# Kernel optimization log

Measured on AMD Instinct MI355X. Metric: run time of the kernel, lower is better.

The kernel has to match this reference:

```python
import jax, jax.numpy as jnp
import numpy as np

H = 12          # num_attention_heads
HD = 64         # head_dim
GAMMA = 0.5
LOCAL_EPS = 0.8
N_APPROX = 7


def _l1norm(x, axis):
    # torch.nn.functional.normalize(x, p=1, dim=axis)
    n = jnp.sum(jnp.abs(x), axis=axis, keepdims=True)
    return x / jnp.maximum(n, 1e-12)


def setup_inputs() -> dict:
    key = jax.random.key(0)
    ks = jax.random.split(key, 6)
    B, S, E = 2, 512, 768
    std = 1.0 / np.sqrt(E)
    hidden_states = jax.random.normal(ks[0], (B, S, E), jnp.float32)
    Wq = jax.random.normal(ks[1], (E, E), jnp.float32) * std
    Wk = jax.random.normal(ks[2], (E, E), jnp.float32) * std
    Wv = jax.random.normal(ks[3], (E, E), jnp.float32) * std
    bq = jnp.zeros((E,), jnp.float32)
    bk = jnp.zeros((E,), jnp.float32)
    bv = jnp.zeros((E,), jnp.float32)
    g = jax.random.randint(ks[4], (B * S, B * S), 0, 2, jnp.int32)
    attention_mask = jnp.zeros((B, S), jnp.float32)
    return {"hidden_states": hidden_states, "Wq": Wq, "bq": bq, "Wk": Wk,
            "bk": bk, "Wv": Wv, "bv": bv, "g": g,
            "attention_mask": attention_mask}


def reference(hidden_states, Wq, bq, Wk, bk, Wv, bv, g, attention_mask):
    B, S, E = hidden_states.shape
    BN = B * S
    x = hidden_states  # torch flattens batch-major: token index = b*S + s
    q = (x @ Wq + bq) / jnp.sqrt(jnp.float32(HD))
    k = x @ Wk + bk
    v = x @ Wv + bv
    # [B,S,E] -> [BN,H,HD] -> [H,BN,HD]
    q = q.reshape(BN, H, HD).transpose(1, 0, 2)
    k = k.reshape(BN, H, HD).transpose(1, 0, 2)
    v = v.reshape(BN, H, HD).transpose(1, 0, 2)

    # W_G[h,i,j] = exp(k_i . q_j)
    W_G = jnp.exp(jnp.einsum('hid,hjd->hij', k, q))

    # sparsification mask combined with token mask
    bool_mask = (attention_mask >= 0).reshape(-1).astype(jnp.int32)  # [BN]
    g_eff = g * (bool_mask[:, None] * bool_mask[None, :])
    W_G = jnp.where(g_eff > 0, W_G, jnp.zeros((), W_G.dtype))

    out_degree = W_G.sum(axis=2)                       # [H, BN]
    rhos = jax.lax.stop_gradient(out_degree.max(axis=1))  # [H]

    eye = jnp.eye(BN, dtype=W_G.dtype)
    Bmat = rhos[:, None, None] * eye + W_G - out_degree[:, :, None] * eye

    B_power = jnp.broadcast_to(eye, (H, BN, BN))
    L_gamma = jnp.broadcast_to(eye, (H, BN, BN))
    num = 1.0
    den = jnp.ones((H,), W_G.dtype)
    for ii in range(1, N_APPROX + 1):  # fixed 7-term power series
        num = num * (GAMMA - ii + 1) * -1.0
        den = den * (ii * rhos)
        coef = num / den                               # [H]
        B_power = jnp.einsum('hij,hjk->hik', Bmat, B_power)
        L_gamma = L_gamma + coef[:, None, None] * B_power
    L_gamma = L_gamma * (rhos[:, None, None] ** GAMMA)
    diags = jnp.diagonal(L_gamma, axis1=-2, axis2=-1)  # [H, BN]
    L_gamma = _l1norm(diags[:, :, None] * eye - L_gamma, axis=2)

    attn = (LOCAL_EPS * jnp.einsum('hij,hjd->hid', _l1norm(W_G, 2), v)
            + (1.0 - LOCAL_EPS) * jnp.einsum('hij,hjd->hid', L_gamma, v))

    # faithful to torch: raw reshape of [H,BN,HD] into [B,S,H,HD]
    out = attn.reshape(B, S, H, HD)
    out = jnp.swapaxes(out, 0, 1).reshape(S, B, E)
    return jnp.swapaxes(out, 0, 1)
```

## Files before the change

kernel.cpp:

```cpp
#include <hip/hip_runtime.h>
#include <hip/hip_bf16.h>

typedef __attribute__((ext_vector_type(4))) float f32x4;
typedef __attribute__((ext_vector_type(8))) short s16x8;

typedef const __attribute__((address_space(1))) void* gptr_t;
typedef __attribute__((address_space(3))) void* lptr_t;

__device__ __forceinline__ short f2b(float f){ __hip_bfloat16 h=__float2bfloat16(f); return *(short*)&h; }
__device__ __forceinline__ float b2f(short s){ __hip_bfloat16 h; *(short*)&h = s; return __bfloat162float(h); }

__device__ __forceinline__ void gl_lds16(const void* g, void* l){
  __builtin_amdgcn_global_load_lds((gptr_t)g, (lptr_t)l, 16, 0, 0);
}


__global__ __launch_bounds__(256) void cvt_x(const float* __restrict__ X, short* __restrict__ Xb){
  int i = blockIdx.x*256 + threadIdx.x;
  const float4* p = (const float4*)(X + (size_t)i*8);
  float4 a = p[0], b = p[1];
  s16x8 o;
  o[0]=f2b(a.x); o[1]=f2b(a.y); o[2]=f2b(a.z); o[3]=f2b(a.w);
  o[4]=f2b(b.x); o[5]=f2b(b.y); o[6]=f2b(b.z); o[7]=f2b(b.w);
  *(s16x8*)(Xb + (size_t)i*8) = o;
}

__global__ __launch_bounds__(256) void cvt_wt3(const float* __restrict__ Wq, const float* __restrict__ Wk,
      const float* __restrict__ Wv, short* __restrict__ WT){
  __shared__ short tile[64][72];
  int mat = blockIdx.x / 144; int bx = blockIdx.x % 144;
  const float* W = mat==0?Wq:(mat==1?Wk:Wv);
  short* O = WT + (size_t)mat*768*768;
  int bl = bx % 12, bn = bx / 12;
  int l0 = bl*64, n0 = bn*64;
  int t = threadIdx.x;
  #pragma unroll
  for (int p=0;p<4;p++){
    int lr = p*16 + (t>>4);
    int nc = (t&15)*4;
    float4 v = *(const float4*)(W + (size_t)(l0+lr)*768 + n0 + nc);
    tile[lr][nc+0]=f2b(v.x); tile[lr][nc+1]=f2b(v.y); tile[lr][nc+2]=f2b(v.z); tile[lr][nc+3]=f2b(v.w);
  }
  __syncthreads();
  #pragma unroll
  for (int p=0;p<2;p++){
    int nr = p*32 + (t>>3);
    int lc = (t&7)*8;
    s16x8 o;
    #pragma unroll
    for(int u=0;u<8;u++) o[u] = tile[lc+u][nr];
    *(s16x8*)(O + (size_t)(n0+nr)*768 + l0 + lc) = o;
  }
}

__global__ __launch_bounds__(256) void gpack(const int* __restrict__ g, unsigned* __restrict__ gb){
  int w = blockIdx.x*256 + threadIdx.x;
  const int* p = g + (size_t)w*32;
  unsigned b=0;
  #pragma unroll
  for(int i=0;i<32;i++) b |= (p[i]>0 ? 1u:0u) << i;
  gb[w]=b;
}

__global__ __launch_bounds__(256) void vtrans(const short* __restrict__ vs, short* __restrict__ vT){
  __shared__ short tile[64][72];
  int h = blockIdx.y; int i0 = blockIdx.x*64;
  int t = threadIdx.x;
  #pragma unroll
  for(int p=0;p<2;p++){
    int ir = p*32 + (t>>3); int c8=(t&7)*8;
    *(s16x8*)&tile[ir][c8] = *(const s16x8*)(vs + (size_t)(i0+ir)*768 + h*64 + c8);
  }
  __syncthreads();
  #pragma unroll
  for(int p=0;p<2;p++){
    int dr = p*32 + (t>>3); int i8=(t&7)*8;
    s16x8 o;
    #pragma unroll
    for(int u=0;u<8;u++) o[u]=tile[i8+u][dr];
    *(s16x8*)(vT + ((size_t)h*64 + dr)*1024 + i0 + i8) = o;
  }
}

__global__ __launch_bounds__(256) void qkv_gemm(const short* __restrict__ Xb, const short* __restrict__ WT,
      const float* __restrict__ bq, const float* __restrict__ bk, const float* __restrict__ bv,
      short* __restrict__ qs, short* __restrict__ ks, short* __restrict__ vs){
  __shared__ short lA[128*32], lB[128*32];
  int mat = blockIdx.y;
  const short* B = WT + (size_t)mat*768*768;
  const float* bias = mat==0?bq:(mat==1?bk:bv);
  short* outp = mat==0?qs:(mat==1?ks:vs);
  float scale = mat==0 ? 0.125f : 1.0f;
  int tm = (blockIdx.x / 6)*128, tn = (blockIdx.x % 6)*128;
  int t=threadIdx.x, wave=t>>6, lane=t&63;
  int srow=t>>2, scol=(t&3)*8;
  int wm=(wave>>1)*64, wn=(wave&1)*64;
  f32x4 acc[4][4]={};
  for (int k0=0;k0<768;k0+=32){
    #pragma unroll
    for(int r=0;r<2;++r){
      gl_lds16(Xb + (size_t)(tm+srow+r*64)*768 + k0 + scol, lA + r*2048 + wave*512);
      gl_lds16(B  + (size_t)(tn+srow+r*64)*768 + k0 + scol, lB + r*2048 + wave*512);
    }
    __syncthreads();
    int krow=(lane>>4)*8, rl=lane&15;
    s16x8 af[4], bfr[4];
    #pragma unroll
    for(int m=0;m<4;m++) af[m] = *(s16x8*)&lA[(wm+m*16+rl)*32 + krow];
    #pragma unroll
    for(int n=0;n<4;n++) bfr[n] = *(s16x8*)&lB[(wn+n*16+rl)*32 + krow];
    #pragma unroll
    for(int m=0;m<4;m++)
      #pragma unroll
      for(int n=0;n<4;n++)
        acc[m][n]=__builtin_amdgcn_mfma_f32_16x16x32_bf16(af[m],bfr[n],acc[m][n],0,0,0);
    __syncthreads();
  }
  int r0 = tm + wm + (lane>>4)*4, c0 = tn + wn + (lane&15);
  #pragma unroll
  for(int m=0;m<4;m++)
    #pragma unroll
    for(int n=0;n<4;n++){
      int col = c0 + n*16; float bb = bias[col];
      #pragma unroll
      for(int r=0;r<4;r++){
        int row = r0 + m*16 + r;
        outp[(size_t)row*768 + col] = f2b((acc[m][n][r] + bb)*scale);
      }
    }
}

__global__ __launch_bounds__(256) void wg_gemm(const short* __restrict__ kb, const short* __restrict__ qb,
      const unsigned* __restrict__ gb, const float* __restrict__ am,
      short* __restrict__ WG, float* __restrict__ od){
  __shared__ short lK[128*64], lQ[128*64];
  int h=blockIdx.y;
  int tm=(blockIdx.x>>3)*128, tn=(blockIdx.x&7)*128;
  int t=threadIdx.x, wave=t>>6, lane=t&63;
  int srow=t>>3, scol=(t&7)*8;
  int wm=(wave>>1)*64, wn=(wave&1)*64;
  #pragma unroll
  for(int r=0;r<4;++r){
    gl_lds16(kb + (size_t)(tm+srow+r*32)*768 + h*64 + scol, lK + r*2048 + wave*512);
    gl_lds16(qb + (size_t)(tn+srow+r*32)*768 + h*64 + scol, lQ + r*2048 + wave*512);
  }
  __syncthreads();
  int rl=lane&15;
  f32x4 acc[4][4]={};
  #pragma unroll
  for(int ks=0;ks<2;ks++){
    int krow=ks*32+(lane>>4)*8;
    s16x8 af[4], bfr[4];
    #pragma unroll
    for(int m=0;m<4;m++) af[m]=*(s16x8*)&lK[(wm+m*16+rl)*64+krow];
    #pragma unroll
    for(int n=0;n<4;n++) bfr[n]=*(s16x8*)&lQ[(wn+n*16+rl)*64+krow];
    #pragma unroll
    for(int m=0;m<4;m++)
      #pragma unroll
      for(int n=0;n<4;n++)
        acc[m][n]=__builtin_amdgcn_mfma_f32_16x16x32_bf16(af[m],bfr[n],acc[m][n],0,0,0);
  }
  size_t hm=(size_t)h<<20;
  int r0=tm+wm+(lane>>4)*4, c0=tn+wn+rl;
  #pragma unroll
  for(int m=0;m<4;m++){
    float rs[4]={0.f,0.f,0.f,0.f};
    #pragma unroll
    for(int n=0;n<4;n++){
      int col=c0+n*16;
      bool mc = am[col] >= 0.0f;
      unsigned sh = col & 31; int wofs = col >> 5;
      #pragma unroll
      for(int r=0;r<4;r++){
        int row=r0+m*16+r;
        float e = __expf(acc[m][n][r]);
        bool gbit = (gb[(row<<5) + wofs] >> sh) & 1u;
        float w = (gbit && am[row]>=0.0f && mc) ? e : 0.f;
        WG[hm+(size_t)row*1024+col]=f2b(w);
        rs[r]+=w;
      }
    }
    #pragma unroll
    for(int r=0;r<4;r++){
      float s=rs[r];
      #pragma unroll
      for(int off=1;off<16;off<<=1) s+=__shfl_xor(s,off);
      if(rl==0) atomicAdd(&od[(h<<10)+r0+m*16+r], s);
    }
  }
}

__global__ void rhos_k(const float* __restrict__ od, float* __restrict__ rhos){
  __shared__ float red[256];
  int h = blockIdx.x, t = threadIdx.x;
  float m = -1e30f;
  for (int i=t;i<1024;i+=256) m = fmaxf(m, od[(h<<10)+i]);
  red[t]=m; __syncthreads();
  for(int s=128;s>0;s>>=1){ if(t<s) red[t]=fmaxf(red[t],red[t+s]); __syncthreads(); }
  if(t==0) rhos[h]=red[0];
}

__global__ __launch_bounds__(256) void amat_t(const short* __restrict__ WG, const float* __restrict__ od,
      const float* __restrict__ rhos, short* __restrict__ Am, short* __restrict__ AmT,
      short* __restrict__ T){
  __shared__ short tile[64][72];
  const float b7 = -33.f/2048.f, b6 = -21.f/1024.f;
  int h = blockIdx.y; int bx = blockIdx.x;
  int rb = bx >> 4, cb = bx & 15;
  int r0 = rb*64, c0 = cb*64;
  float rho = rhos[h]; float inv = 1.0f/fmaxf(rho,1e-30f);
  size_t hm = (size_t)h<<20;
  int t = threadIdx.x;
  #pragma unroll
  for(int p=0;p<2;p++){
    int r = p*32 + (t>>3); int c8 = (t&7)*8;
    size_t base = hm + (size_t)(r0+r)*1024 + c0 + c8;
    s16x8 w = *(const s16x8*)(WG + base);
    s16x8 oa, ot;
    float dadd = (rho - od[(h<<10)+r0+r])*inv;
    #pragma unroll
    for(int u=0;u<8;u++){
      bool dg = (rb==cb) && ((c8+u)==r);
      float a = b2f(w[u])*inv + (dg ? dadd : 0.f);
      oa[u]=f2b(a);
      ot[u]=f2b(b7*a + (dg ? b6 : 0.f));
      tile[r][c8+u]=oa[u];
    }
    *(s16x8*)(Am+base)=oa; *(s16x8*)(T+base)=ot;
  }
  __syncthreads();
  #pragma unroll
  for(int p=0;p<2;p++){
    int c = p*32 + (t>>3); int r8 = (t&7)*8;
    s16x8 o;
    #pragma unroll
    for(int u=0;u<8;u++) o[u]=tile[r8+u][c];
    *(s16x8*)(AmT + hm + (size_t)(c0+c)*1024 + r0 + r8) = o;
  }
}

#define GEMM2P_PROLOG \
  __shared__ short lA[2][4096], lB[2][4096]; \
  int wg = ((int)blockIdx.x & 7)*96 + ((int)blockIdx.x >> 3); \
  int h = wg >> 6; int tile = wg & 63; \
  int tm=(tile>>3)*128, tn=(tile&7)*128; \
  size_t hm=(size_t)h<<20; \
  const short* Ag = A + hm; const short* Bg = B + hm; \
  int t=threadIdx.x, wave=t>>6, lane=t&63; \
  int srow=t>>2, scol=(t&3)*8; \
  int wm=(wave>>1)*64, wn=(wave&1)*64; \
  int krow=(lane>>4)*8, rl=lane&15; \
  const short* pA0 = Ag + (size_t)(tm+srow)*1024 + scol; \
  const short* pA1 = pA0 + (size_t)64*1024; \
  const short* pB0 = Bg + (size_t)(tn+srow)*1024 + scol; \
  const short* pB1 = pB0 + (size_t)64*1024; \
  f32x4 acc[4][4]={}; \
  gl_lds16(pA0, &lA[0][wave*512]); \
  gl_lds16(pA1, &lA[0][2048 + wave*512]); \
  gl_lds16(pB0, &lB[0][wave*512]); \
  gl_lds16(pB1, &lB[0][2048 + wave*512]); \
  pA0+=32; pA1+=32; pB0+=32; pB1+=32; \
  __syncthreads(); \
  int cur=0; \
  _Pragma("unroll 1") \
  for(int k0=32;k0<1024;k0+=32){ \
    gl_lds16(pA0, &lA[cur^1][wave*512]); \
    gl_lds16(pA1, &lA[cur^1][2048 + wave*512]); \
    gl_lds16(pB0, &lB[cur^1][wave*512]); \
    gl_lds16(pB1, &lB[cur^1][2048 + wave*512]); \
    pA0+=32; pA1+=32; pB0+=32; pB1+=32; \
    s16x8 af[4], bfr[4]; \
    _Pragma("unroll") \
    for(int m=0;m<4;m++) af[m]=*(s16x8*)&lA[cur][(wm+m*16+rl)*32+krow]; \
    _Pragma("unroll") \
    for(int n=0;n<4;n++) bfr[n]=*(s16x8*)&lB[cur][(wn+n*16+rl)*32+krow]; \
    __builtin_amdgcn_s_setprio(1); \
    _Pragma("unroll") \
    for(int m=0;m<4;m++) \
      _Pragma("unroll") \
      for(int n=0;n<4;n++) \
        acc[m][n]=__builtin_amdgcn_mfma_f32_16x16x32_bf16(af[m],bfr[n],acc[m][n],0,0,0); \
    __builtin_amdgcn_s_setprio(0); \
    __syncthreads(); \
    cur^=1; \
  } \
  { s16x8 af[4], bfr[4]; \
    _Pragma("unroll") \
    for(int m=0;m<4;m++) af[m]=*(s16x8*)&lA[cur][(wm+m*16+rl)*32+krow]; \
    _Pragma("unroll") \
    for(int n=0;n<4;n++) bfr[n]=*(s16x8*)&lB[cur][(wn+n*16+rl)*32+krow]; \
    __builtin_amdgcn_s_setprio(1); \
    _Pragma("unroll") \
    for(int m=0;m<4;m++) \
      _Pragma("unroll") \
      for(int n=0;n<4;n++) \
        acc[m][n]=__builtin_amdgcn_mfma_f32_16x16x32_bf16(af[m],bfr[n],acc[m][n],0,0,0); \
    __builtin_amdgcn_s_setprio(0); \
  } \
  int r0=tm+wm+(lane>>4)*4, c0=tn+wn+(lane&15);

__global__ __launch_bounds__(256) void gemm2p_plain(const short* __restrict__ A, const short* __restrict__ B,
      short* __restrict__ D){
  GEMM2P_PROLOG
  short* Dg = D + hm;
  #pragma unroll
  for(int m=0;m<4;m++)
    #pragma unroll
    for(int n=0;n<4;n++){
      int col=c0+n*16;
      #pragma unroll
      for(int r=0;r<4;r++)
        Dg[(size_t)(r0+m*16+r)*1024 + col]=f2b(acc[m][n][r]);
    }
}

__global__ __launch_bounds__(256) void gemm2p_epi(const short* __restrict__ A, const short* __restrict__ B,
      short* __restrict__ D, const short* __restrict__ E1, const short* __restrict__ E2,
      float c0c, float cA, float cB){
  GEMM2P_PROLOG
  short* Dg = D + hm;
  const short* E1g = E1 + hm; const short* E2g = E2 + hm;
  #pragma unroll
  for(int m=0;m<4;m++)
    #pragma unroll
    for(int n=0;n<4;n++){
      int col=c0+n*16;
      #pragma unroll
      for(int r=0;r<4;r++){
        int row=r0+m*16+r;
        size_t e = (size_t)row*1024 + col;
        float v = acc[m][n][r] + cA*b2f(E1g[e]) + cB*b2f(E2g[e]);
        if(row==col) v += c0c;
        Dg[e]=f2b(v);
      }
    }
}

__global__ __launch_bounds__(256) void gemm2p_epi_stat(const short* __restrict__ A, const short* __restrict__ B,
      short* __restrict__ D, const short* __restrict__ E1, const short* __restrict__ E2,
      float c0c, float cA, float cB, float* __restrict__ rowabs, float* __restrict__ dvp){
  GEMM2P_PROLOG
  short* Dg = D + hm;
  const short* E1g = E1 + hm; const short* E2g = E2 + hm;
  #pragma unroll
  for(int m=0;m<4;m++){
    float rs[4]={0.f,0.f,0.f,0.f};
    #pragma unroll
    for(int n=0;n<4;n++){
      int col=c0+n*16;
      #pragma unroll
      for(int r=0;r<4;r++){
        int row=r0+m*16+r;
        size_t e = (size_t)row*1024 + col;
        float v = acc[m][n][r] + cA*b2f(E1g[e]) + cB*b2f(E2g[e]);
        if(row==col){ v += c0c; dvp[(h<<10)+row] = v; }
        rs[r] += fabsf(v);
        Dg[e]=f2b(v);
      }
    }
    #pragma unroll
    for(int r=0;r<4;r++){
      float s=rs[r];
      #pragma unroll
      for(int off=1;off<16;off<<=1) s+=__shfl_xor(s,off);
      if(rl==0) atomicAdd(&rowabs[(h<<10)+r0+m*16+r], s);
    }
  }
}

__global__ __launch_bounds__(256) void attn_k(const short* __restrict__ WG, const short* __restrict__ L,
    const short* __restrict__ vT, const short* __restrict__ vs,
    const float* __restrict__ od, const float* __restrict__ dv, const float* __restrict__ rowabs,
    float* __restrict__ out){
  __shared__ short lW[64*32], lL[64*32], lV[64*32];
  int h=blockIdx.y, tm=blockIdx.x*64;
  size_t hm=(size_t)h<<20;
  int t=threadIdx.x, wave=t>>6, lane=t&63;
  int srow=t>>2, scol=(t&3)*8;
  f32x4 a1[4]={}, a2[4]={};
  for(int j0=0;j0<1024;j0+=32){
    gl_lds16(WG + hm + (size_t)(tm+srow)*1024 + j0 + scol, lW + wave*512);
    gl_lds16(L  + hm + (size_t)(tm+srow)*1024 + j0 + scol, lL + wave*512);
    gl_lds16(vT + ((size_t)h*64 + srow)*1024 + j0 + scol, lV + wave*512);
    __syncthreads();
    int krow=(lane>>4)*8, rl=lane&15;
    s16x8 fw, fl, fv[4];
    fw=*(s16x8*)&lW[(wave*16+rl)*32+krow];
    fl=*(s16x8*)&lL[(wave*16+rl)*32+krow];
    #pragma unroll
    for(int n=0;n<4;n++) fv[n]=*(s16x8*)&lV[(n*16+rl)*32+krow];
    #pragma unroll
    for(int n=0;n<4;n++){
      a1[n]=__builtin_amdgcn_mfma_f32_16x16x32_bf16(fw,fv[n],a1[n],0,0,0);
      a2[n]=__builtin_amdgcn_mfma_f32_16x16x32_bf16(fl,fv[n],a2[n],0,0,0);
    }
    __syncthreads();
  }
  #pragma unroll
  for(int r=0;r<4;r++){
    int row = tm + wave*16 + (lane>>4)*4 + r;
    float invod = 1.0f/fmaxf(od[(h<<10)+row], 1e-12f);
    float dvi = dv[(h<<10)+row];
    float ivr = 1.0f/fmaxf(rowabs[(h<<10)+row] - fabsf(dvi), 1e-12f);
    #pragma unroll
    for(int n=0;n<4;n++){
      int d = n*16 + (lane&15);
      float vv = b2f(vs[(size_t)row*768 + h*64 + d]);
      out[(((size_t)h<<10)+row)*64 + d] = 0.8f*a1[n][r]*invod + 0.2f*(dvi*vv - a2[n][r])*ivr;
    }
  }
}

extern "C" void kernel_launch(void* const* d_in, const int* in_sizes, int n_in,
                              void* d_out, int out_size, void* d_ws, size_t ws_size,
                              hipStream_t stream){
  const float* hs = (const float*)d_in[0];
  const float* Wq = (const float*)d_in[1];
  const float* bq = (const float*)d_in[2];
  const float* Wk = (const float*)d_in[3];
  const float* bk = (const float*)d_in[4];
  const float* Wv = (const float*)d_in[5];
  const float* bv = (const float*)d_in[6];
  const int*   g  = (const int*)d_in[7];
  const float* am = (const float*)d_in[8];
  float* out = (float*)d_out;

  char* w = (char*)d_ws;
  auto alloc=[&](size_t bytes)->char*{ char* p=w; w += (bytes+255)&~(size_t)255; return p; };
  short* Xb  = (short*)alloc((size_t)1024*768*2);
  short* WT  = (short*)alloc((size_t)3*768*768*2);
  short* qs  = (short*)alloc((size_t)1024*768*2);
  short* ks  = (short*)alloc((size_t)1024*768*2);
  short* vs  = (short*)alloc((size_t)1024*768*2);
  short* vT  = (short*)alloc((size_t)12*64*1024*2);
  unsigned* gb = (unsigned*)alloc((size_t)1024*32*4);
  short* WG  = (short*)alloc((size_t)12*1024*1024*2);
  short* Am  = (short*)alloc((size_t)12*1024*1024*2);
  short* AmT = (short*)alloc((size_t)12*1024*1024*2);
  short* Tm  = (short*)alloc((size_t)12*1024*1024*2);
  short* A2  = (short*)alloc((size_t)12*1024*1024*2);
  short* A3T = (short*)alloc((size_t)12*1024*1024*2);
  float* od  = (float*)alloc((size_t)2*12*1024*4);
  float* rab = od + 12*1024;
  float* rh  = (float*)alloc((size_t)64*4);
  float* dv  = (float*)alloc((size_t)12*1024*4);

  hipMemsetAsync(od, 0, (size_t)2*12*1024*4, stream);

  cvt_x<<<384,256,0,stream>>>(hs, Xb);
  cvt_wt3<<<432,256,0,stream>>>(Wq, Wk, Wv, WT);
  gpack<<<128,256,0,stream>>>(g, gb);
  qkv_gemm<<<dim3(48,3),256,0,stream>>>(Xb, WT, bq,bk,bv, qs,ks,vs);
  vtrans<<<dim3(16,12),256,0,stream>>>(vs, vT);
  wg_gemm<<<dim3(64,12),256,0,stream>>>(ks, qs, gb, am, WG, od);
  rhos_k<<<12,256,0,stream>>>(od, rh);
  amat_t<<<dim3(256,12),256,0,stream>>>(WG, od, rh, Am, AmT, Tm);

  const float b1=-0.5f, b2=-0.125f, b3=-1.f/16.f, b4=-5.f/128.f, b5=-7.f/256.f;
  short* V = AmT;
  short* L = Tm;
  gemm2p_plain<<<768,256,0,stream>>>(Am, AmT, A2);
  gemm2p_plain<<<768,256,0,stream>>>(AmT, A2, A3T);
  gemm2p_epi<<<768,256,0,stream>>>(Tm, A3T, V, Am, A2, b3,b4,b5);
  gemm2p_epi_stat<<<768,256,0,stream>>>(V, A3T, L, Am, A2, 1.0f,b1,b2, rab, dv);

  attn_k<<<dim3(16,12),256,0,stream>>>(WG, L, vT, vs, od, dv, rab, out);
}
```

Measured before the change: 280.8 us.

## Merge prep kernels into one launch and double-buffer QKV GEMM loads

Folds the three preprocessing kernels (x conversion, weight transpose-convert, mask bit-packing) into a single launch that branches on block index, which saves two kernel launches. Separately, the QKV GEMM now uses double-buffered LDS so the direct global-to-LDS loads for the next K-slice are issued before the MFMAs on the current slice, and it raises wave priority around the MFMA block. The prep kernel's __syncthreads sits inside a branch, but the branch is uniform per block so this is safe. Doubling LDS per block may reduce occupancy.

Result: no change. 280.8 us, median of 2 (-0.0%).

```diff
diff --git a/kernel.cpp b/kernel.cpp
--- a/kernel.cpp
+++ b/kernel.cpp
@@ -14,52 +14,51 @@
   __builtin_amdgcn_global_load_lds((gptr_t)g, (lptr_t)l, 16, 0, 0);
 }
 
-
-__global__ __launch_bounds__(256) void cvt_x(const float* __restrict__ X, short* __restrict__ Xb){
-  int i = blockIdx.x*256 + threadIdx.x;
-  const float4* p = (const float4*)(X + (size_t)i*8);
-  float4 a = p[0], b = p[1];
-  s16x8 o;
-  o[0]=f2b(a.x); o[1]=f2b(a.y); o[2]=f2b(a.z); o[3]=f2b(a.w);
-  o[4]=f2b(b.x); o[5]=f2b(b.y); o[6]=f2b(b.z); o[7]=f2b(b.w);
-  *(s16x8*)(Xb + (size_t)i*8) = o;
-}
-
-__global__ __launch_bounds__(256) void cvt_wt3(const float* __restrict__ Wq, const float* __restrict__ Wk,
-      const float* __restrict__ Wv, short* __restrict__ WT){
+__global__ __launch_bounds__(256) void prep_all(const float* __restrict__ X, short* __restrict__ Xb,
+      const float* __restrict__ Wq, const float* __restrict__ Wk, const float* __restrict__ Wv,
+      short* __restrict__ WT, const int* __restrict__ g, unsigned* __restrict__ gb){
   __shared__ short tile[64][72];
-  int mat = blockIdx.x / 144; int bx = blockIdx.x % 144;
-  const float* W = mat==0?Wq:(mat==1?Wk:Wv);
-  short* O = WT + (size_t)mat*768*768;
-  int bl = bx % 12, bn = bx / 12;
-  int l0 = bl*64, n0 = bn*64;
-  int t = threadIdx.x;
-  #pragma unroll
-  for (int p=0;p<4;p++){
-    int lr = p*16 + (t>>4);
-    int nc = (t&15)*4;
-    float4 v = *(const float4*)(W + (size_t)(l0+lr)*768 + n0 + nc);
-    tile[lr][nc+0]=f2b(v.x); tile[lr][nc+1]=f2b(v.y); tile[lr][nc+2]=f2b(v.z); tile[lr][nc+3]=f2b(v.w);
-  }
-  __syncthreads();
-  #pragma unroll
-  for (int p=0;p<2;p++){
-    int nr = p*32 + (t>>3);
-    int lc = (t&7)*8;
+  int b = blockIdx.x; int t = threadIdx.x;
+  if (b < 384){
+    int i = b*256 + t;
+    const float4* p = (const float4*)(X + (size_t)i*8);
+    float4 a = p[0], c = p[1];
     s16x8 o;
-    #pragma unroll
-    for(int u=0;u<8;u++) o[u] = tile[lc+u][nr];
-    *(s16x8*)(O + (size_t)(n0+nr)*768 + l0 + lc) = o;
-  }
-}
-
-__global__ __launch_bounds__(256) void gpack(const int* __restrict__ g, unsigned* __restrict__ gb){
-  int w = blockIdx.x*256 + threadIdx.x;
-  const int* p = g + (size_t)w*32;
-  unsigned b=0;
-  #pragma unroll
-  for(int i=0;i<32;i++) b |= (p[i]>0 ? 1u:0u) << i;
-  gb[w]=b;
+    o[0]=f2b(a.x); o[1]=f2b(a.y); o[2]=f2b(a.z); o[3]=f2b(a.w);
+    o[4]=f2b(c.x); o[5]=f2b(c.y); o[6]=f2b(c.z); o[7]=f2b(c.w);
+    *(s16x8*)(Xb + (size_t)i*8) = o;
+  } else if (b < 816){
+    int bx2 = b - 384;
+    int mat = bx2 / 144; int bx = bx2 % 144;
+    const float* W = mat==0?Wq:(mat==1?Wk:Wv);
+    short* O = WT + (size_t)mat*768*768;
+    int bl = bx % 12, bn = bx / 12;
+    int l0 = bl*64, n0 = bn*64;
+    #pragma unroll
+    for (int p=0;p<4;p++){
+      int lr = p*16 + (t>>4);
+      int nc = (t&15)*4;
+      float4 v = *(const float4*)(W + (size_t)(l0+lr)*768 + n0 + nc);
+      tile[lr][nc+0]=f2b(v.x); tile[lr][nc+1]=f2b(v.y); tile[lr][nc+2]=f2b(v.z); tile[lr][nc+3]=f2b(v.w);
+    }
+    __syncthreads();
+    #pragma unroll
+    for (int p=0;p<2;p++){
+      int nr = p*32 + (t>>3);
+      int lc = (t&7)*8;
+      s16x8 o;
+      #pragma unroll
+      for(int u=0;u<8;u++) o[u] = tile[lc+u][nr];
+      *(s16x8*)(O + (size_t)(n0+nr)*768 + l0 + lc) = o;
+    }
+  } else {
+    int w = (b-816)*256 + t;
+    const int* p = g + (size_t)w*32;
+    unsigned bm=0;
+    #pragma unroll
+    for(int i=0;i<32;i++) bm |= (p[i]>0 ? 1u:0u) << i;
+    gb[w]=bm;
+  }
 }
 
 __global__ __launch_bounds__(256) void vtrans(const short* __restrict__ vs, short* __restrict__ vT){
@@ -85,7 +84,7 @@
 __global__ __launch_bounds__(256) void qkv_gemm(const short* __restrict__ Xb, const short* __restrict__ WT,
       const float* __restrict__ bq, const float* __restrict__ bk, const float* __restrict__ bv,
       short* __restrict__ qs, short* __restrict__ ks, short* __restrict__ vs){
-  __shared__ short lA[128*32], lB[128*32];
+  __shared__ short lA[2][4096], lB[2][4096];
   int mat = blockIdx.y;
   const short* B = WT + (size_t)mat*768*768;
   const float* bias = mat==0?bq:(mat==1?bk:bv);
@@ -95,26 +94,53 @@
   int t=threadIdx.x, wave=t>>6, lane=t&63;
   int srow=t>>2, scol=(t&3)*8;
   int wm=(wave>>1)*64, wn=(wave&1)*64;
+  int krow=(lane>>4)*8, rl=lane&15;
+  const short* pA0 = Xb + (size_t)(tm+srow)*768 + scol;
+  const short* pA1 = pA0 + (size_t)64*768;
+  const short* pB0 = B + (size_t)(tn+srow)*768 + scol;
+  const short* pB1 = pB0 + (size_t)64*768;
   f32x4 acc[4][4]={};
-  for (int k0=0;k0<768;k0+=32){
-    #pragma unroll
-    for(int r=0;r<2;++r){
-      gl_lds16(Xb + (size_t)(tm+srow+r*64)*768 + k0 + scol, lA + r*2048 + wave*512);
-      gl_lds16(B  + (size_t)(tn+srow+r*64)*768 + k0 + scol, lB + r*2048 + wave*512);
-    }
-    __syncthreads();
-    int krow=(lane>>4)*8, rl=lane&15;
+  gl_lds16(pA0, &lA[0][wave*512]);
+  gl_lds16(pA1, &lA[0][2048 + wave*512]);
+  gl_lds16(pB0, &lB[0][wave*512]);
+  gl_lds16(pB1, &lB[0][2048 + wave*512]);
+  pA0+=32; pA1+=32; pB0+=32; pB1+=32;
+  __syncthreads();
+  int cur=0;
+  #pragma unroll 1
+  for (int k0=32;k0<768;k0+=32){
+    gl_lds16(pA0, &lA[cur^1][wave*512]);
+    gl_lds16(pA1, &lA[cur^1][2048 + wave*512]);
+    gl_lds16(pB0, &lB[cur^1][wave*512]);
+    gl_lds16(pB1, &lB[cur^1][2048 + wave*512]);
+    pA0+=32; pA1+=32; pB0+=32; pB1+=32;
     s16x8 af[4], bfr[4];
     #pragma unroll
-    for(int m=0;m<4;m++) af[m] = *(s16x8*)&lA[(wm+m*16+rl)*32 + krow];
-    #pragma unroll
-    for(int n=0;n<4;n++) bfr[n] = *(s16x8*)&lB[(wn+n*16+rl)*32 + krow];
+    for(int m=0;m<4;m++) af[m] = *(s16x8*)&lA[cur][(wm+m*16+rl)*32 + krow];
+    #pragma unroll
+    for(int n=0;n<4;n++) bfr[n] = *(s16x8*)&lB[cur][(wn+n*16+rl)*32 + krow];
+    __builtin_amdgcn_s_setprio(1);
     #pragma unroll
     for(int m=0;m<4;m++)
       #pragma unroll
       for(int n=0;n<4;n++)
         acc[m][n]=__builtin_amdgcn_mfma_f32_16x16x32_bf16(af[m],bfr[n],acc[m][n],0,0,0);
+    __builtin_amdgcn_s_setprio(0);
     __syncthreads();
+    cur^=1;
+  }
+  { s16x8 af[4], bfr[4];
+    #pragma unroll
+    for(int m=0;m<4;m++) af[m] = *(s16x8*)&lA[cur][(wm+m*16+rl)*32 + krow];
+    #pragma unroll
+    for(int n=0;n<4;n++) bfr[n] = *(s16x8*)&lB[cur][(wn+n*16+rl)*32 + krow];
+    __builtin_amdgcn_s_setprio(1);
+    #pragma unroll
+    for(int m=0;m<4;m++)
+      #pragma unroll
+      for(int n=0;n<4;n++)
+        acc[m][n]=__builtin_amdgcn_mfma_f32_16x16x32_bf16(af[m],bfr[n],acc[m][n],0,0,0);
+    __builtin_amdgcn_s_setprio(0);
   }
   int r0 = tm + wm + (lane>>4)*4, c0 = tn + wn + (lane&15);
   #pragma unroll
@@ -448,9 +474,7 @@
 
   hipMemsetAsync(od, 0, (size_t)2*12*1024*4, stream);
 
-  cvt_x<<<384,256,0,stream>>>(hs, Xb);
-  cvt_wt3<<<432,256,0,stream>>>(Wq, Wk, Wv, WT);
-  gpack<<<128,256,0,stream>>>(g, gb);
+  prep_all<<<944,256,0,stream>>>(hs, Xb, Wq, Wk, Wv, WT, g, gb);
   qkv_gemm<<<dim3(48,3),256,0,stream>>>(Xb, WT, bq,bk,bv, qs,ks,vs);
   vtrans<<<dim3(16,12),256,0,stream>>>(vs, vT);
   wg_gemm<<<dim3(64,12),256,0,stream>>>(ks, qs, gb, am, WG, od);
```
